# Optimization experiments

Hardware: AMD Instinct MI355X
Metric: run time of the kernel (lower is better)

The kernel has to match this reference:

```python
import jax, jax.numpy as jnp
import numpy as np

EPS = 1e-8  # matches PairwiseCosine eps clamp


def setup_inputs() -> dict:
    key = jax.random.key(0)
    k1, k2, k3 = jax.random.split(key, 3)
    B, N, M, D = 8, 2048, 2048, 256
    desc_src = jax.random.normal(k1, (B, N, D), dtype=jnp.float32)
    desc_dst = jax.random.normal(k2, (B, M, D), dtype=jnp.float32)
    points_dst = jax.random.uniform(k3, (B, M, 2), dtype=jnp.float32)
    return {"desc_src": desc_src, "desc_dst": desc_dst, "points_dst": points_dst}


def reference(desc_src, desc_dst, points_dst):
    # Pairwise cosine similarity: [B, N, M]
    xx = jnp.linalg.norm(desc_src, axis=-1, keepdims=True)          # [B, N, 1]
    yy = jnp.linalg.norm(desc_dst, axis=-1, keepdims=True)          # [B, M, 1]
    xy = jnp.einsum('bnd,bmd->bnm', desc_src, desc_dst)             # [B, N, M]
    sim = xy / jnp.maximum(xx * jnp.swapaxes(yy, 1, 2), EPS)
    # Best match per source descriptor
    confidence = jnp.max(sim, axis=2)                               # [B, N]
    idx = jnp.argmax(sim, axis=2)                                   # [B, N]
    # Gather matched destination points: [B, N, 2]
    matched = jnp.take_along_axis(points_dst, idx[:, :, None], axis=1)
    return (matched, confidence)
```

## Files before the change

kernel.cpp:

```cpp
#include <hip/hip_runtime.h>
#include <stdint.h>

constexpr int Bq = 8, Nq = 2048, Mq = 2048, Dq = 256;
constexpr int TILE = 128;
constexpr int KC = 32;
constexpr int NCH = Dq / KC;
constexpr int LDS_S = 40;

typedef float f32x4 __attribute__((ext_vector_type(4)));
typedef _Float16 f16x8 __attribute__((ext_vector_type(8)));
typedef _Float16 f16x4 __attribute__((ext_vector_type(4)));
typedef __fp16 fp16x2 __attribute__((ext_vector_type(2)));

__device__ __forceinline__ uint32_t f2sortable(float f) {
  uint32_t u = __float_as_uint(f);
  return (u & 0x80000000u) ? ~u : (u | 0x80000000u);
}
__device__ __forceinline__ float sortable2f(uint32_t s) {
  uint32_t u = (s & 0x80000000u) ? (s ^ 0x80000000u) : ~s;
  return __uint_as_float(u);
}

__device__ __forceinline__ void load16(float* d, const float* __restrict__ p) {
  *(float4*)&d[0]  = *(const float4*)(p + 0);
  *(float4*)&d[4]  = *(const float4*)(p + 4);
  *(float4*)&d[8]  = *(const float4*)(p + 8);
  *(float4*)&d[12] = *(const float4*)(p + 12);
}

__device__ __forceinline__ void split8(const float* x, f16x8* hi, f16x8* lo,
                                       float& sq) {
  union { f16x8 v; fp16x2 p[4]; } H, L;
#pragma unroll
  for (int j = 0; j < 4; ++j) {
    float x0 = x[2 * j], x1 = x[2 * j + 1];
    sq = fmaf(x0, x0, sq);
    sq = fmaf(x1, x1, sq);
    float h0 = __uint_as_float(__float_as_uint(x0) & 0xFFFFE000u);
    float h1 = __uint_as_float(__float_as_uint(x1) & 0xFFFFE000u);
    H.p[j] = __builtin_amdgcn_cvt_pkrtz(h0, h1);
    L.p[j] = __builtin_amdgcn_cvt_pkrtz(x0 - h0, x1 - h1);
  }
  *hi = H.v;
  *lo = L.v;
}


__global__ __launch_bounds__(256)
void prep_kernel(const float* __restrict__ src, const float* __restrict__ dst,
                 _Float16* __restrict__ Ah, _Float16* __restrict__ Al,
                 _Float16* __restrict__ Bh, _Float16* __restrict__ Bl,
                 float* __restrict__ invnx, float* __restrict__ invny) {
  const int lane = threadIdx.x & 63;
  const int wv = threadIdx.x >> 6;
  const int r = blockIdx.x * 4 + wv;

  const float* x;
  _Float16 *h, *l;
  float* inv;
  if (blockIdx.y == 0) { x = src; h = Ah; l = Al; inv = invnx; }
  else                 { x = dst; h = Bh; l = Bl; inv = invny; }

  float4 v = *(const float4*)(x + (size_t)r * Dq + lane * 4);
  float sq = 0.f;
  union { f16x4 v; fp16x2 p[2]; } H, L;
  float e[4] = {v.x, v.y, v.z, v.w};
#pragma unroll
  for (int j = 0; j < 2; ++j) {
    float x0 = e[2 * j], x1 = e[2 * j + 1];
    sq = fmaf(x0, x0, sq);
    sq = fmaf(x1, x1, sq);
    float h0 = __uint_as_float(__float_as_uint(x0) & 0xFFFFE000u);
    float h1 = __uint_as_float(__float_as_uint(x1) & 0xFFFFE000u);
    H.p[j] = __builtin_amdgcn_cvt_pkrtz(h0, h1);
    L.p[j] = __builtin_amdgcn_cvt_pkrtz(x0 - h0, x1 - h1);
  }
#pragma unroll
  for (int m = 1; m <= 32; m <<= 1) sq += __shfl_xor(sq, m);

  const int b = r >> 11, row = r & 2047;
  const int c = lane >> 3, ko = (lane & 7) * 4;
  size_t idx = ((size_t)(b * NCH + c) * 2048 + row) * KC + ko;
  *(f16x4*)&h[idx] = H.v;
  *(f16x4*)&l[idx] = L.v;
  if (lane == 0) inv[r] = 1.0f / sqrtf(sq);
}

__device__ __forceinline__ void stage(const _Float16* g, _Float16* l, int lane) {
  const char* gc = (const char*)g + lane * 16;
  char* lc = (char*)l;
#pragma unroll
  for (int i = 0; i < 8; ++i)
    __builtin_amdgcn_global_load_lds(
        (const __attribute__((address_space(1))) void*)(gc + i * 1024),
        (__attribute__((address_space(3))) void*)(lc + i * 1024),
        16, 0, 0);
}

__global__ __launch_bounds__(256, 2)
void simmax_mfma(const _Float16* __restrict__ Ah, const _Float16* __restrict__ Al,
                 const _Float16* __restrict__ Bh, const _Float16* __restrict__ Bl,
                 const float* __restrict__ invnx, const float* __restrict__ invny,
                 unsigned long long* __restrict__ best) {
  __shared__ __align__(16) _Float16 lds[2][4][TILE][KC];

  const int b = blockIdx.z, nt = blockIdx.y, mt = blockIdx.x;
  const int tid = threadIdx.x;
  const int lane = tid & 63;
  const int wave = tid >> 6;
  const int wy = wave >> 1, wx = wave & 1;
  const int ln15 = lane & 15, lq = lane >> 4;

  const _Float16* garr = (wave == 0) ? Ah : (wave == 1) ? Al
                        : (wave == 2) ? Bh : Bl;
  const int grow = ((wave < 2) ? nt : mt) * TILE;
  const _Float16* g0 = garr + ((size_t)(b * NCH) * 2048 + grow) * KC;
  constexpr size_t CSTR = (size_t)2048 * KC;

  f32x4 acc[4][4];
#pragma unroll
  for (int i = 0; i < 4; ++i)
#pragma unroll
    for (int j = 0; j < 4; ++j) acc[i][j] = (f32x4){0.f, 0.f, 0.f, 0.f};

  stage(g0, &lds[0][wave][0][0], lane);
  __syncthreads();

#pragma unroll
  for (int c = 0; c < NCH; ++c) {
    const int cb = c & 1;
    if (c + 1 < NCH)
      stage(g0 + (size_t)(c + 1) * CSTR, &lds[cb ^ 1][wave][0][0], lane);

    f16x8 bhf[4], blf[4];
#pragma unroll
    for (int ct = 0; ct < 4; ++ct) {
      const int rb = wx * 64 + ct * 16 + ln15;
      bhf[ct] = *(const f16x8*)&lds[cb][2][rb][lq * 8];
      blf[ct] = *(const f16x8*)&lds[cb][3][rb][lq * 8];
    }
#pragma unroll
    for (int rt = 0; rt < 4; ++rt) {
      const int ra = wy * 64 + rt * 16 + ln15;
      f16x8 ahf = *(const f16x8*)&lds[cb][0][ra][lq * 8];
      f16x8 alf = *(const f16x8*)&lds[cb][1][ra][lq * 8];
#pragma unroll
      for (int ct = 0; ct < 4; ++ct) {
        acc[rt][ct] = __builtin_amdgcn_mfma_f32_16x16x32_f16(ahf, bhf[ct], acc[rt][ct], 0, 0, 0);
        acc[rt][ct] = __builtin_amdgcn_mfma_f32_16x16x32_f16(ahf, blf[ct], acc[rt][ct], 0, 0, 0);
        acc[rt][ct] = __builtin_amdgcn_mfma_f32_16x16x32_f16(alf, bhf[ct], acc[rt][ct], 0, 0, 0);
      }
    }
    if (c + 1 < NCH) __syncthreads();
  }

  float invy[4];
#pragma unroll
  for (int ct = 0; ct < 4; ++ct)
    invy[ct] = invny[(size_t)b * Mq + mt * TILE + wx * 64 + ct * 16 + ln15];

#pragma unroll
  for (int rt = 0; rt < 4; ++rt) {
#pragma unroll
    for (int reg = 0; reg < 4; ++reg) {
      float bq = -1e30f;
      int bc = 0x7FFFFFFF;
#pragma unroll
      for (int ct = 0; ct < 4; ++ct) {
        float q = acc[rt][ct][reg] * invy[ct];
        int cg = mt * TILE + wx * 64 + ct * 16 + ln15;
        if (q > bq || (q == bq && cg < bc)) { bq = q; bc = cg; }
      }
#pragma unroll
      for (int m = 1; m <= 8; m <<= 1) {
        float q2 = __shfl_xor(bq, m);
        int c2 = __shfl_xor(bc, m);
        if (q2 > bq || (q2 == bq && c2 < bc)) { bq = q2; bc = c2; }
      }
      if (ln15 == 0) {
        int rloc = wy * 64 + rt * 16 + lq * 4 + reg;
        float conf = bq * invnx[(size_t)b * Nq + nt * TILE + rloc];
        unsigned long long p =
            ((unsigned long long)(f2sortable(conf) ^ 0x80000000u) << 32) |
            (uint32_t)(~(uint32_t)bc);
        atomicMax((long long*)&best[(size_t)b * Nq + nt * TILE + rloc],
                  (long long)p);
      }
    }
  }
}

__global__ __launch_bounds__(256, 3)
void simmax_kernel(const float* __restrict__ src, const float* __restrict__ dst,
                   unsigned long long* __restrict__ best) {
  __shared__ _Float16 Ah[TILE][LDS_S], Al[TILE][LDS_S];
  __shared__ _Float16 Bh[TILE][LDS_S], Bl[TILE][LDS_S];
  __shared__ float invnx_s[TILE], invny_s[TILE];

  const int b = blockIdx.z, nt = blockIdx.y, mt = blockIdx.x;
  const int tid = threadIdx.x;
  const int lane = tid & 63;
  const int wave = tid >> 6;
  const int wy = wave >> 1, wx = wave & 1;
  const int ln15 = lane & 15, lq = lane >> 4;

  const int sr = tid >> 1;
  const int sk = (tid & 1) * 16;
  const float* Ag = src + ((size_t)(b * Nq + nt * TILE + sr)) * Dq + sk;
  const float* Bg = dst + ((size_t)(b * Mq + mt * TILE + sr)) * Dq + sk;

  f32x4 acc[4][4];
#pragma unroll
  for (int i = 0; i < 4; ++i)
#pragma unroll
    for (int j = 0; j < 4; ++j) acc[i][j] = (f32x4){0.f, 0.f, 0.f, 0.f};
  float sqa = 0.f, sqb = 0.f;

  float av[16], bv[16];
  load16(av, Ag);
  load16(bv, Bg);

  for (int c = 0; c < NCH; ++c) {
    f16x8 ah2[2], al2[2], bh2[2], bl2[2];
    split8(&av[0], &ah2[0], &al2[0], sqa);
    split8(&av[8], &ah2[1], &al2[1], sqa);
    split8(&bv[0], &bh2[0], &bl2[0], sqb);
    split8(&bv[8], &bh2[1], &bl2[1], sqb);
    __syncthreads();
    *(f16x8*)&Ah[sr][sk]     = ah2[0];
    *(f16x8*)&Ah[sr][sk + 8] = ah2[1];
    *(f16x8*)&Al[sr][sk]     = al2[0];
    *(f16x8*)&Al[sr][sk + 8] = al2[1];
    *(f16x8*)&Bh[sr][sk]     = bh2[0];
    *(f16x8*)&Bh[sr][sk + 8] = bh2[1];
    *(f16x8*)&Bl[sr][sk]     = bl2[0];
    *(f16x8*)&Bl[sr][sk + 8] = bl2[1];
    __syncthreads();

    if (c + 1 < NCH) {
      load16(av, Ag + (c + 1) * KC);
      load16(bv, Bg + (c + 1) * KC);
    }

    f16x8 bhf[4], blf[4];
#pragma unroll
    for (int ct = 0; ct < 4; ++ct) {
      int rowb = wx * 64 + ct * 16 + ln15;
      bhf[ct] = *(const f16x8*)&Bh[rowb][lq * 8];
      blf[ct] = *(const f16x8*)&Bl[rowb][lq * 8];
    }
#pragma unroll
    for (int rt = 0; rt < 4; ++rt) {
      int rowa = wy * 64 + rt * 16 + ln15;
      f16x8 ahf = *(const f16x8*)&Ah[rowa][lq * 8];
      f16x8 alf = *(const f16x8*)&Al[rowa][lq * 8];
#pragma unroll
      for (int ct = 0; ct < 4; ++ct) {
        acc[rt][ct] = __builtin_amdgcn_mfma_f32_16x16x32_f16(ahf, bhf[ct], acc[rt][ct], 0, 0, 0);
        acc[rt][ct] = __builtin_amdgcn_mfma_f32_16x16x32_f16(ahf, blf[ct], acc[rt][ct], 0, 0, 0);
        acc[rt][ct] = __builtin_amdgcn_mfma_f32_16x16x32_f16(alf, bhf[ct], acc[rt][ct], 0, 0, 0);
      }
    }
  }

  sqa += __shfl_xor(sqa, 1);
  sqb += __shfl_xor(sqb, 1);
  if ((tid & 1) == 0) {
    invnx_s[sr] = 1.0f / sqrtf(sqa);
    invny_s[sr] = 1.0f / sqrtf(sqb);
  }
  __syncthreads();

  float invny[4];
#pragma unroll
  for (int ct = 0; ct < 4; ++ct) invny[ct] = invny_s[wx * 64 + ct * 16 + ln15];

#pragma unroll
  for (int rt = 0; rt < 4; ++rt) {
#pragma unroll
    for (int reg = 0; reg < 4; ++reg) {
      float bq = -1e30f;
      int bc = 0x7FFFFFFF;
#pragma unroll
      for (int ct = 0; ct < 4; ++ct) {
        float q = acc[rt][ct][reg] * invny[ct];
        int cg = mt * TILE + wx * 64 + ct * 16 + ln15;
        if (q > bq || (q == bq && cg < bc)) { bq = q; bc = cg; }
      }
#pragma unroll
      for (int m = 1; m <= 8; m <<= 1) {
        float q2 = __shfl_xor(bq, m);
        int c2 = __shfl_xor(bc, m);
        if (q2 > bq || (q2 == bq && c2 < bc)) { bq = q2; bc = c2; }
      }
      if (ln15 == 0) {
        int rloc = wy * 64 + rt * 16 + lq * 4 + reg;
        float conf = bq * invnx_s[rloc];
        unsigned long long p =
            ((unsigned long long)(f2sortable(conf) ^ 0x80000000u) << 32) |
            (uint32_t)(~(uint32_t)bc);
        atomicMax((long long*)&best[(size_t)b * Nq + nt * TILE + rloc],
                  (long long)p);
      }
    }
  }
}

__global__ void finalize_kernel(const unsigned long long* __restrict__ best,
                                const float* __restrict__ pts,
                                float* __restrict__ out) {
  int i = blockIdx.x * blockDim.x + threadIdx.x;
  if (i >= Bq * Nq) return;
  unsigned long long p = best[i];
  uint32_t s = (uint32_t)(p >> 32) ^ 0x80000000u;
  int idx = (int)(~(uint32_t)(p & 0xFFFFFFFFull));
  float conf = sortable2f(s);
  int b = i / Nq;
  const float* q = pts + ((size_t)b * Mq + (size_t)idx) * 2;
  out[(size_t)i * 2 + 0] = q[0];
  out[(size_t)i * 2 + 1] = q[1];
  out[(size_t)(Bq * Nq) * 2 + i] = conf;
}

extern "C" void kernel_launch(void* const* d_in, const int* in_sizes, int n_in,
                              void* d_out, int out_size, void* d_ws, size_t ws_size,
                              hipStream_t stream) {
  const float* src = (const float*)d_in[0];
  const float* dst = (const float*)d_in[1];
  const float* pts = (const float*)d_in[2];
  float* out = (float*)d_out;

  unsigned long long* best = (unsigned long long*)d_ws;

  constexpr size_t BEST_B = (size_t)Bq * Nq * 8;
  constexpr size_t HL_B   = (size_t)Bq * 2048 * Dq * 2;
  constexpr size_t INV_B  = (size_t)Bq * 2048 * 4;
  constexpr size_t NEED   = BEST_B + 4 * HL_B + 2 * INV_B;

  if (ws_size >= NEED) {
    uint8_t* w = (uint8_t*)d_ws + BEST_B;
    _Float16* Ah = (_Float16*)(w);
    _Float16* Al = (_Float16*)(w + 1 * HL_B);
    _Float16* Bh = (_Float16*)(w + 2 * HL_B);
    _Float16* Bl = (_Float16*)(w + 3 * HL_B);
    float* invnx = (float*)(w + 4 * HL_B);
    float* invny = (float*)(w + 4 * HL_B + INV_B);

    prep_kernel<<<dim3(4096, 2, 1), 256, 0, stream>>>(src, dst, Ah, Al, Bh, Bl,
                                                      invnx, invny);
    simmax_mfma<<<dim3(Mq / TILE, Nq / TILE, Bq), 256, 0, stream>>>(
        Ah, Al, Bh, Bl, invnx, invny, best);
  } else {
    simmax_kernel<<<dim3(Mq / TILE, Nq / TILE, Bq), 256, 0, stream>>>(src, dst,
                                                                      best);
  }
  {
    int blocks = (Bq * Nq + 255) / 256;
    finalize_kernel<<<blocks, 256, 0, stream>>>(best, pts, out);
  }
}
```

Baseline: 176.5 us.

## Load MFMA fragments directly from global into registers, drop LDS staging

Replaces the LDS double-buffered staging of hi/lo fp16 tiles with direct global-to-register fragment loads, software-pipelined across two register sets, and removes all block-level barriers. It also remaps the flat block index so that consecutive blocks are spread across batches, which is meant to improve L2/XCD locality. The trade-off is that each wave now loads its own A and B fragments from global/L2 with no sharing through LDS, so cache traffic roughly doubles and register pressure rises from holding two fragment sets.

```diff
diff --git a/kernel.cpp b/kernel.cpp
--- a/kernel.cpp
+++ b/kernel.cpp
@@ -86,36 +86,60 @@
   if (lane == 0) inv[r] = 1.0f / sqrtf(sq);
 }
 
-__device__ __forceinline__ void stage(const _Float16* g, _Float16* l, int lane) {
-  const char* gc = (const char*)g + lane * 16;
-  char* lc = (char*)l;
-#pragma unroll
-  for (int i = 0; i < 8; ++i)
-    __builtin_amdgcn_global_load_lds(
-        (const __attribute__((address_space(1))) void*)(gc + i * 1024),
-        (__attribute__((address_space(3))) void*)(lc + i * 1024),
-        16, 0, 0);
+
+constexpr size_t CSTR = (size_t)2048 * KC;
+
+struct FragSet { f16x8 ah[4], al[4], bh[4], bl[4]; };
+
+__device__ __forceinline__ void load_set(const _Float16* __restrict__ Abh,
+                                         const _Float16* __restrict__ Abl,
+                                         const _Float16* __restrict__ Bbh,
+                                         const _Float16* __restrict__ Bbl,
+                                         int c, FragSet& s) {
+#pragma unroll
+  for (int t = 0; t < 4; ++t) {
+    const size_t off = (size_t)c * CSTR + (size_t)t * 16 * KC;
+    s.ah[t] = *(const f16x8*)(Abh + off);
+    s.al[t] = *(const f16x8*)(Abl + off);
+    s.bh[t] = *(const f16x8*)(Bbh + off);
+    s.bl[t] = *(const f16x8*)(Bbl + off);
+  }
+}
+
+__device__ __forceinline__ void mfma_set(const FragSet& s, f32x4 acc[4][4]) {
+#pragma unroll
+  for (int rt = 0; rt < 4; ++rt)
+#pragma unroll
+    for (int ct = 0; ct < 4; ++ct) {
+      acc[rt][ct] = __builtin_amdgcn_mfma_f32_16x16x32_f16(s.ah[rt], s.bh[ct], acc[rt][ct], 0, 0, 0);
+      acc[rt][ct] = __builtin_amdgcn_mfma_f32_16x16x32_f16(s.ah[rt], s.bl[ct], acc[rt][ct], 0, 0, 0);
+      acc[rt][ct] = __builtin_amdgcn_mfma_f32_16x16x32_f16(s.al[rt], s.bh[ct], acc[rt][ct], 0, 0, 0);
+    }
 }
 
 __global__ __launch_bounds__(256, 2)
-void simmax_mfma(const _Float16* __restrict__ Ah, const _Float16* __restrict__ Al,
-                 const _Float16* __restrict__ Bh, const _Float16* __restrict__ Bl,
-                 const float* __restrict__ invnx, const float* __restrict__ invny,
-                 unsigned long long* __restrict__ best) {
-  __shared__ __align__(16) _Float16 lds[2][4][TILE][KC];
-
-  const int b = blockIdx.z, nt = blockIdx.y, mt = blockIdx.x;
+void simmax_reg(const _Float16* __restrict__ Ah, const _Float16* __restrict__ Al,
+                const _Float16* __restrict__ Bh, const _Float16* __restrict__ Bl,
+                const float* __restrict__ invnx, const float* __restrict__ invny,
+                unsigned long long* __restrict__ best) {
+  const int orig = blockIdx.x;
+  const int logical = (orig & 7) * 256 + (orig >> 3);
+  const int b = logical >> 8;
+  const int nt = (logical >> 4) & 15;
+  const int mt = logical & 15;
+
   const int tid = threadIdx.x;
   const int lane = tid & 63;
   const int wave = tid >> 6;
   const int wy = wave >> 1, wx = wave & 1;
   const int ln15 = lane & 15, lq = lane >> 4;
 
-  const _Float16* garr = (wave == 0) ? Ah : (wave == 1) ? Al
-                        : (wave == 2) ? Bh : Bl;
-  const int grow = ((wave < 2) ? nt : mt) * TILE;
-  const _Float16* g0 = garr + ((size_t)(b * NCH) * 2048 + grow) * KC;
-  constexpr size_t CSTR = (size_t)2048 * KC;
+  const size_t rbA = ((size_t)(b * NCH) * 2048 + nt * TILE + wy * 64 + ln15) * KC + lq * 8;
+  const size_t rbB = ((size_t)(b * NCH) * 2048 + mt * TILE + wx * 64 + ln15) * KC + lq * 8;
+  const _Float16* Abh = Ah + rbA;
+  const _Float16* Abl = Al + rbA;
+  const _Float16* Bbh = Bh + rbB;
+  const _Float16* Bbl = Bl + rbB;
 
   f32x4 acc[4][4];
 #pragma unroll
@@ -123,35 +147,15 @@
 #pragma unroll
     for (int j = 0; j < 4; ++j) acc[i][j] = (f32x4){0.f, 0.f, 0.f, 0.f};
 
-  stage(g0, &lds[0][wave][0][0], lane);
-  __syncthreads();
-
-#pragma unroll
-  for (int c = 0; c < NCH; ++c) {
-    const int cb = c & 1;
-    if (c + 1 < NCH)
-      stage(g0 + (size_t)(c + 1) * CSTR, &lds[cb ^ 1][wave][0][0], lane);
-
-    f16x8 bhf[4], blf[4];
-#pragma unroll
-    for (int ct = 0; ct < 4; ++ct) {
-      const int rb = wx * 64 + ct * 16 + ln15;
-      bhf[ct] = *(const f16x8*)&lds[cb][2][rb][lq * 8];
-      blf[ct] = *(const f16x8*)&lds[cb][3][rb][lq * 8];
-    }
-#pragma unroll
-    for (int rt = 0; rt < 4; ++rt) {
-      const int ra = wy * 64 + rt * 16 + ln15;
-      f16x8 ahf = *(const f16x8*)&lds[cb][0][ra][lq * 8];
-      f16x8 alf = *(const f16x8*)&lds[cb][1][ra][lq * 8];
-#pragma unroll
-      for (int ct = 0; ct < 4; ++ct) {
-        acc[rt][ct] = __builtin_amdgcn_mfma_f32_16x16x32_f16(ahf, bhf[ct], acc[rt][ct], 0, 0, 0);
-        acc[rt][ct] = __builtin_amdgcn_mfma_f32_16x16x32_f16(ahf, blf[ct], acc[rt][ct], 0, 0, 0);
-        acc[rt][ct] = __builtin_amdgcn_mfma_f32_16x16x32_f16(alf, bhf[ct], acc[rt][ct], 0, 0, 0);
-      }
-    }
-    if (c + 1 < NCH) __syncthreads();
+  FragSet s0, s1;
+  load_set(Abh, Abl, Bbh, Bbl, 0, s0);
+#pragma unroll
+  for (int cc = 0; cc < NCH; cc += 2) {
+    load_set(Abh, Abl, Bbh, Bbl, cc + 1, s1);
+    mfma_set(s0, acc);
+    if (cc + 2 < NCH)
+      load_set(Abh, Abl, Bbh, Bbl, cc + 2, s0);
+    mfma_set(s1, acc);
   }
 
   float invy[4];
@@ -348,8 +352,8 @@
 
     prep_kernel<<<dim3(4096, 2, 1), 256, 0, stream>>>(src, dst, Ah, Al, Bh, Bl,
                                                       invnx, invny);
-    simmax_mfma<<<dim3(Mq / TILE, Nq / TILE, Bq), 256, 0, stream>>>(
-        Ah, Al, Bh, Bl, invnx, invny, best);
+    simmax_reg<<<dim3(2048, 1, 1), 256, 0, stream>>>(Ah, Al, Bh, Bl,
+                                                     invnx, invny, best);
   } else {
     simmax_kernel<<<dim3(Mq / TILE, Nq / TILE, Bq), 256, 0, stream>>>(src, dst,
                                                                       best);
```

Measured after the change: 166.8 us. 5.5% less time.
